# Kernel optimization log

Measured on AMD Instinct MI355X. Metric: run time of the kernel, lower is better.

## Reference

```python
import jax, jax.numpy as jnp
import numpy as np


def _conv1x1(x, w, b):
    # x: [B, Cin, H, W]; w: [Cout, Cin, 1, 1]; b: [Cout]
    y = jnp.einsum('bchw,oc->bohw', x, w[:, :, 0, 0])
    return y + b[None, :, None, None]


def setup_inputs() -> dict:
    key = jax.random.key(0)
    ks = jax.random.split(key, 9)
    B, C, H, W = 8, 256, 64, 64
    Cq = C // 4
    sc = 0.05
    return {
        'x': jax.random.normal(ks[0], (B, C, H, W), jnp.float32),
        'query_weight': jax.random.normal(ks[1], (Cq, C, 1, 1), jnp.float32) * sc,
        'query_bias': jax.random.normal(ks[2], (Cq,), jnp.float32) * sc,
        'key_weight': jax.random.normal(ks[3], (Cq, C, 1, 1), jnp.float32) * sc,
        'key_bias': jax.random.normal(ks[4], (Cq,), jnp.float32) * sc,
        'value_weight': jax.random.normal(ks[5], (C, C, 1, 1), jnp.float32) * sc,
        'value_bias': jax.random.normal(ks[6], (C,), jnp.float32) * sc,
        'gamma_weight': jax.random.normal(ks[7], (C, C, 1, 1), jnp.float32) * sc,
        'gamma_bias': jax.random.normal(ks[8], (C,), jnp.float32) * sc,
    }


def reference(x, query_weight, query_bias, key_weight, key_bias,
              value_weight, value_bias, gamma_weight, gamma_bias):
    B, C, H, W = x.shape
    N = H * W
    q = _conv1x1(x, query_weight, query_bias).reshape(B, -1, N)   # [B, Cq, N]
    k = _conv1x1(x, key_weight, key_bias).reshape(B, -1, N)       # [B, Cq, N]
    v = _conv1x1(x, value_weight, value_bias).reshape(B, C, N)    # [B, C, N]
    # energy[b, i, j] = sum_c q[b, c, i] * k[b, c, j]
    energy = jnp.einsum('bci,bcj->bij', q, k)                     # [B, N, N]
    energy = jax.nn.elu(energy) / N
    out = jnp.einsum('bcn,bnm->bcm', v, energy).reshape(B, C, H, W)
    return _conv1x1(out, gamma_weight, gamma_bias)
```

## Files before the change

### kernel.cpp

```cpp
#include <hip/hip_runtime.h>
#include <cmath>

#define BB 8
#define CC 256
#define CQ 64
#define NN 4096
constexpr float INV_N = 1.0f / 4096.0f;

typedef __attribute__((ext_vector_type(8))) short short8;
typedef __attribute__((ext_vector_type(4))) short short4v;
typedef __attribute__((ext_vector_type(4))) float float4v;

__device__ __forceinline__ short f2bf(float f) {
  union { float f; unsigned u; } x; x.f = f;
  unsigned r = x.u + 0x7fffu + ((x.u >> 16) & 1u);
  return (short)(r >> 16);
}

__device__ __forceinline__ void lds_barrier() {
  asm volatile("s_waitcnt lgkmcnt(0)" ::: "memory");
  __builtin_amdgcn_s_barrier();
  __builtin_amdgcn_sched_barrier(0);
}

__global__ void wconv_kernel(const float* __restrict__ wq,
                             const float* __restrict__ wk,
                             const float* __restrict__ wv,
                             const float* __restrict__ wg,
                             short* __restrict__ wqb, short* __restrict__ wkb,
                             short* __restrict__ wvb, short* __restrict__ wgb) {
  const int t = blockIdx.x * 256 + threadIdx.x;
  const float* src;
  short* dst;
  int idx;
  if (t < 4096)        { src = wq; dst = wqb; idx = t; }
  else if (t < 8192)   { src = wk; dst = wkb; idx = t - 4096; }
  else if (t < 24576)  { src = wv; dst = wvb; idx = t - 8192; }
  else                 { src = wg; dst = wgb; idx = t - 24576; }
  const float4 v = *reinterpret_cast<const float4*>(&src[(size_t)idx * 4]);
  short4v o;
  o[0] = f2bf(v.x); o[1] = f2bf(v.y); o[2] = f2bf(v.z); o[3] = f2bf(v.w);
  *reinterpret_cast<short4v*>(&dst[(size_t)idx * 4]) = o;
}

__global__ __launch_bounds__(256, 2) void qkv_kernel(
    const float* __restrict__ X,
    const short* __restrict__ wqb, const float* __restrict__ bq,
    const short* __restrict__ wkb, const float* __restrict__ bk,
    const short* __restrict__ wvb, const float* __restrict__ bv,
    short* __restrict__ qt, short* __restrict__ kt, short* __restrict__ vbf) {
  __shared__ short xt[64 * 264];
  const int tid = threadIdx.x;
  const int wid = tid >> 6;
  const int lane = tid & 63, quad = lane >> 4, l16 = lane & 15;
  const int b = blockIdx.x, n0 = blockIdx.y * 64;

  float4 xb[16];
#pragma unroll
  for (int p = 0; p < 16; ++p) {
    const int idx = p * 256 + tid;
    const int c = idx >> 4;
    const int n4 = (idx & 15) * 4;
    xb[p] = *reinterpret_cast<const float4*>(
        &X[((size_t)b * CC + c) * NN + n0 + n4]);
  }
#pragma unroll
  for (int p = 0; p < 16; ++p) {
    const int idx = p * 256 + tid;
    const int c = idx >> 4;
    const int n4 = (idx & 15) * 4;
    xt[(n4 + 0) * 264 + c] = f2bf(xb[p].x);
    xt[(n4 + 1) * 264 + c] = f2bf(xb[p].y);
    xt[(n4 + 2) * 264 + c] = f2bf(xb[p].z);
    xt[(n4 + 3) * 264 + c] = f2bf(xb[p].w);
  }
  __syncthreads();

  short8 bfr[8][4];
#pragma unroll
  for (int kk = 0; kk < 8; ++kk)
#pragma unroll
    for (int tm = 0; tm < 4; ++tm)
      bfr[kk][tm] = *reinterpret_cast<const short8*>(
          &xt[(tm * 16 + l16) * 264 + kk * 32 + quad * 8]);
  __syncthreads();

  short* Os0 = xt;
  short* Os1 = xt + 4608;

  for (int ch = 0; ch < 6; ++ch) {
    const short* W; const float* bias; int obase;
    if (ch == 0)      { W = wqb; bias = bq; obase = 0; }
    else if (ch == 1) { W = wkb; bias = bk; obase = 0; }
    else { W = wvb + (size_t)(ch - 2) * 64 * CC; bias = bv + (ch - 2) * 64; obase = (ch - 2) * 64; }

    const short* wrow = &W[(size_t)(wid * 16 + l16) * CC + quad * 8];
    short8 wf[8];
#pragma unroll
    for (int kk = 0; kk < 8; ++kk)
      wf[kk] = *reinterpret_cast<const short8*>(wrow + kk * 32);

    float4v acc[4];
#pragma unroll
    for (int tm = 0; tm < 4; ++tm) acc[tm] = float4v{0.f, 0.f, 0.f, 0.f};
#pragma unroll
    for (int kk = 0; kk < 8; ++kk)
#pragma unroll
      for (int tm = 0; tm < 4; ++tm)
        acc[tm] = __builtin_amdgcn_mfma_f32_16x16x32_bf16(wf[kk], bfr[kk][tm], acc[tm], 0, 0, 0);

    if (ch < 2) {
      short* dst = (ch == 0) ? qt : kt;
#pragma unroll
      for (int tm = 0; tm < 4; ++tm) {
        short4v pk;
#pragma unroll
        for (int r = 0; r < 4; ++r)
          pk[r] = f2bf(acc[tm][r] + bias[wid * 16 + quad * 4 + r]);
        *reinterpret_cast<short4v*>(
            &dst[((size_t)b * NN + n0 + tm * 16 + l16) * 64 + wid * 16 + quad * 4]) = pk;
      }
    } else {
      short* Os = (ch & 1) ? Os1 : Os0;
#pragma unroll
      for (int tm = 0; tm < 4; ++tm)
#pragma unroll
        for (int r = 0; r < 4; ++r)
          Os[(wid * 16 + quad * 4 + r) * 72 + tm * 16 + l16] =
              f2bf(acc[tm][r] + bias[wid * 16 + quad * 4 + r]);
      __syncthreads();
      const int o = tid >> 2, ng = (tid & 3) * 16;
      const short8 s0 = *reinterpret_cast<const short8*>(&Os[o * 72 + ng]);
      const short8 s1 = *reinterpret_cast<const short8*>(&Os[o * 72 + ng + 8]);
      short* vp = &vbf[((size_t)b * CC + obase + o) * NN + n0 + ng];
      *reinterpret_cast<short8*>(vp) = s0;
      *reinterpret_cast<short8*>(vp + 8) = s1;
    }
  }
}

__global__ __launch_bounds__(256, 2) void attn_kernel(
    const short* __restrict__ qt, const short* __restrict__ kt,
    const short* __restrict__ vbf, const short* __restrict__ wgb,
    const float* __restrict__ bg, float* __restrict__ out) {
  __shared__ short smem[16896];
  short* Es0 = smem;
  short* Es1 = smem + 4608;
  short* Outs = smem;

  const int tid = threadIdx.x;
  const int wid = tid >> 6;
  const int lane = tid & 63, quad = lane >> 4, l16 = lane & 15;
  const int b = blockIdx.x, m0 = blockIdx.y * 64;

  short8 bkf[4][2];
#pragma unroll
  for (int tm = 0; tm < 4; ++tm)
#pragma unroll
    for (int kk = 0; kk < 2; ++kk)
      bkf[tm][kk] = *reinterpret_cast<const short8*>(
          &kt[((size_t)b * NN + m0 + tm * 16 + l16) * 64 + kk * 32 + quad * 8]);

  const short* qp = &qt[((size_t)b * NN + wid * 16 + l16) * 64 + quad * 8];
  const short* vrow[4];
#pragma unroll
  for (int tc = 0; tc < 4; ++tc)
    vrow[tc] = &vbf[((size_t)b * CC + wid * 64 + tc * 16 + l16) * NN + quad * 8];

  float4v acc[4][4];
#pragma unroll
  for (int i = 0; i < 4; ++i)
#pragma unroll
    for (int j = 0; j < 4; ++j) acc[i][j] = float4v{0.f, 0.f, 0.f, 0.f};

  short8 avA[4][2], avB[4][2];
#pragma unroll
  for (int tc = 0; tc < 4; ++tc) {
    avA[tc][0] = *reinterpret_cast<const short8*>(vrow[tc]);
    avA[tc][1] = *reinterpret_cast<const short8*>(vrow[tc] + 32);
  }
  short8 aqA0 = *reinterpret_cast<const short8*>(qp + (size_t)1 * 4096);
  short8 aqA1 = *reinterpret_cast<const short8*>(qp + (size_t)1 * 4096 + 32);
  short8 aqB0, aqB1;
  {
    const short8 aq0 = *reinterpret_cast<const short8*>(qp);
    const short8 aq1 = *reinterpret_cast<const short8*>(qp + 32);
#pragma unroll
    for (int tm = 0; tm < 4; ++tm) {
      float4v t = {0.f, 0.f, 0.f, 0.f};
      t = __builtin_amdgcn_mfma_f32_16x16x32_bf16(aq0, bkf[tm][0], t, 0, 0, 0);
      t = __builtin_amdgcn_mfma_f32_16x16x32_bf16(aq1, bkf[tm][1], t, 0, 0, 0);
      short4v pk;
#pragma unroll
      for (int r = 0; r < 4; ++r) {
        float sv = t[r];
        sv = (sv > 0.f) ? sv : (__expf(sv) - 1.f);
        pk[r] = f2bf(sv);
      }
      *reinterpret_cast<short4v*>(
          &Es0[(tm * 16 + l16) * 72 + wid * 16 + quad * 4]) = pk;
    }
  }
  lds_barrier();

  auto seg = [&](int it, short8 (&avc)[4][2], short8 (&avn)[4][2],
                 short8& aqc0, short8& aqc1, short8& aqn0, short8& aqn1) {
    const int nb1 = (it + 1) * 64;
#pragma unroll
    for (int tc = 0; tc < 4; ++tc) {
      avn[tc][0] = *reinterpret_cast<const short8*>(vrow[tc] + nb1);
      avn[tc][1] = *reinterpret_cast<const short8*>(vrow[tc] + nb1 + 32);
    }
    aqn0 = *reinterpret_cast<const short8*>(qp + (size_t)(it + 2) * 4096);
    aqn1 = *reinterpret_cast<const short8*>(qp + (size_t)(it + 2) * 4096 + 32);

    short* Esr = (it & 1) ? Es1 : Es0;
    short* Esw = (it & 1) ? Es0 : Es1;

    float4v s[4];
    if (it < 63) {
#pragma unroll
      for (int tm = 0; tm < 4; ++tm) {
        float4v t = {0.f, 0.f, 0.f, 0.f};
        t = __builtin_amdgcn_mfma_f32_16x16x32_bf16(aqc0, bkf[tm][0], t, 0, 0, 0);
        t = __builtin_amdgcn_mfma_f32_16x16x32_bf16(aqc1, bkf[tm][1], t, 0, 0, 0);
        s[tm] = t;
      }
    }

#pragma unroll
    for (int tm = 0; tm < 4; ++tm) {
      const short8 be0 = *reinterpret_cast<const short8*>(
          &Esr[(tm * 16 + l16) * 72 + quad * 8]);
      const short8 be1 = *reinterpret_cast<const short8*>(
          &Esr[(tm * 16 + l16) * 72 + 32 + quad * 8]);
#pragma unroll
      for (int tc = 0; tc < 4; ++tc) {
        acc[tc][tm] = __builtin_amdgcn_mfma_f32_16x16x32_bf16(avc[tc][0], be0, acc[tc][tm], 0, 0, 0);
        acc[tc][tm] = __builtin_amdgcn_mfma_f32_16x16x32_bf16(avc[tc][1], be1, acc[tc][tm], 0, 0, 0);
      }
    }

    if (it < 63) {
#pragma unroll
      for (int tm = 0; tm < 4; ++tm) {
        short4v pk;
#pragma unroll
        for (int r = 0; r < 4; ++r) {
          float sv = s[tm][r];
          sv = (sv > 0.f) ? sv : (__expf(sv) - 1.f);
          pk[r] = f2bf(sv);
        }
        *reinterpret_cast<short4v*>(
            &Esw[(tm * 16 + l16) * 72 + wid * 16 + quad * 4]) = pk;
      }
    }
    lds_barrier();
  };

  for (int it = 0; it < 64; it += 2) {
    seg(it,     avA, avB, aqA0, aqA1, aqB0, aqB1);
    seg(it + 1, avB, avA, aqB0, aqB1, aqA0, aqA1);
  }

#pragma unroll
  for (int tc = 0; tc < 4; ++tc)
#pragma unroll
    for (int tm = 0; tm < 4; ++tm) {
      short4v pk;
#pragma unroll
      for (int r = 0; r < 4; ++r) pk[r] = f2bf(acc[tc][tm][r] * INV_N);
      *reinterpret_cast<short4v*>(
          &Outs[(tm * 16 + l16) * 264 + wid * 64 + tc * 16 + quad * 4]) = pk;
    }
  __syncthreads();

#pragma unroll
  for (int i = 0; i < 4; ++i)
#pragma unroll
    for (int j = 0; j < 4; ++j) acc[i][j] = float4v{0.f, 0.f, 0.f, 0.f};

  for (int ks8 = 0; ks8 < 8; ++ks8) {
    short8 ag[4];
#pragma unroll
    for (int to = 0; to < 4; ++to)
      ag[to] = *reinterpret_cast<const short8*>(
          &wgb[(size_t)(wid * 64 + to * 16 + l16) * CC + ks8 * 32 + quad * 8]);
    short8 bo[4];
#pragma unroll
    for (int tm = 0; tm < 4; ++tm)
      bo[tm] = *reinterpret_cast<const short8*>(
          &Outs[(tm * 16 + l16) * 264 + ks8 * 32 + quad * 8]);
#pragma unroll
    for (int to = 0; to < 4; ++to)
#pragma unroll
      for (int tm = 0; tm < 4; ++tm)
        acc[to][tm] =
            __builtin_amdgcn_mfma_f32_16x16x32_bf16(ag[to], bo[tm], acc[to][tm], 0, 0, 0);
  }

#pragma unroll
  for (int to = 0; to < 4; ++to) {
#pragma unroll
    for (int r = 0; r < 4; ++r) {
      const int o = wid * 64 + to * 16 + quad * 4 + r;
      const float bgv = bg[o];
#pragma unroll
      for (int tm = 0; tm < 4; ++tm) {
        out[((size_t)b * CC + o) * NN + m0 + tm * 16 + l16] =
            acc[to][tm][r] + bgv;
      }
    }
  }
}

extern "C" void kernel_launch(void* const* d_in, const int* in_sizes, int n_in,
                              void* d_out, int out_size, void* d_ws,
                              size_t ws_size, hipStream_t stream) {
  const float* x  = (const float*)d_in[0];
  const float* wq = (const float*)d_in[1];
  const float* bq = (const float*)d_in[2];
  const float* wk = (const float*)d_in[3];
  const float* bk = (const float*)d_in[4];
  const float* wv = (const float*)d_in[5];
  const float* bv = (const float*)d_in[6];
  const float* wg = (const float*)d_in[7];
  const float* bg = (const float*)d_in[8];
  float* out = (float*)d_out;

  short* qt  = (short*)d_ws;
  short* kt  = qt + (size_t)BB * NN * CQ;
  short* vbf = kt + (size_t)BB * NN * CQ;
  short* wqb = vbf + (size_t)BB * CC * NN;
  short* wkb = wqb + (size_t)CQ * CC;
  short* wvb = wkb + (size_t)CQ * CC;
  short* wgb = wvb + (size_t)CC * CC;

  wconv_kernel<<<dim3(160), 256, 0, stream>>>(wq, wk, wv, wg, wqb, wkb, wvb, wgb);
  qkv_kernel<<<dim3(BB, NN / 64), 256, 0, stream>>>(x, wqb, bq, wkb, bk, wvb, bv,
                                                    qt, kt, vbf);
  attn_kernel<<<dim3(BB, NN / 64), 256, 0, stream>>>(qt, kt, vbf, wgb, bg, out);
}
```

Measured before the change: 270.0 us.

## Fold gamma projection into value weights and pad V row stride

Precomputes Wg·Wv and Wg·bv in a new prep kernel so the value projection directly produces gamma-projected values. This removes the trailing 1x1 gamma GEMM and its LDS staging from the attention kernel, leaving only scaling and bias at output. The V buffer row stride is also padded to 4224 to reduce memory conflicts on strided row reads. It adds a small extra launch and changes rounding because the combined weight is quantised to bf16.

Measured after the change: 274.7 us. About the same (+1.7%).

```diff
diff --git a/kernel.cpp b/kernel.cpp
--- a/kernel.cpp
+++ b/kernel.cpp
@@ -5,6 +5,7 @@
 #define CC 256
 #define CQ 64
 #define NN 4096
+#define VROW 4224
 constexpr float INV_N = 1.0f / 4096.0f;
 
 typedef __attribute__((ext_vector_type(8))) short short8;
@@ -25,29 +26,42 @@
 
 __global__ void wconv_kernel(const float* __restrict__ wq,
                              const float* __restrict__ wk,
-                             const float* __restrict__ wv,
-                             const float* __restrict__ wg,
-                             short* __restrict__ wqb, short* __restrict__ wkb,
-                             short* __restrict__ wvb, short* __restrict__ wgb) {
+                             short* __restrict__ wqb, short* __restrict__ wkb) {
   const int t = blockIdx.x * 256 + threadIdx.x;
-  const float* src;
-  short* dst;
-  int idx;
-  if (t < 4096)        { src = wq; dst = wqb; idx = t; }
-  else if (t < 8192)   { src = wk; dst = wkb; idx = t - 4096; }
-  else if (t < 24576)  { src = wv; dst = wvb; idx = t - 8192; }
-  else                 { src = wg; dst = wgb; idx = t - 24576; }
+  const float* src; short* dst; int idx;
+  if (t < 4096) { src = wq; dst = wqb; idx = t; }
+  else          { src = wk; dst = wkb; idx = t - 4096; }
   const float4 v = *reinterpret_cast<const float4*>(&src[(size_t)idx * 4]);
   short4v o;
   o[0] = f2bf(v.x); o[1] = f2bf(v.y); o[2] = f2bf(v.z); o[3] = f2bf(v.w);
   *reinterpret_cast<short4v*>(&dst[(size_t)idx * 4]) = o;
 }
 
+__global__ void wprep_kernel(const float* __restrict__ wg,
+                             const float* __restrict__ wv,
+                             const float* __restrict__ bv,
+                             short* __restrict__ wvpb, float* __restrict__ bvp) {
+  const int o = blockIdx.x, t = threadIdx.x;
+  float s = 0.f;
+  for (int c = 0; c < 256; ++c)
+    s += wg[(size_t)o * 256 + c] * wv[(size_t)c * 256 + t];
+  wvpb[(size_t)o * 256 + t] = f2bf(s);
+
+  __shared__ float red[256];
+  red[t] = wg[(size_t)o * 256 + t] * bv[t];
+  __syncthreads();
+  for (int off = 128; off; off >>= 1) {
+    if (t < off) red[t] += red[t + off];
+    __syncthreads();
+  }
+  if (t == 0) bvp[o] = red[0];
+}
+
 __global__ __launch_bounds__(256, 2) void qkv_kernel(
     const float* __restrict__ X,
     const short* __restrict__ wqb, const float* __restrict__ bq,
     const short* __restrict__ wkb, const float* __restrict__ bk,
-    const short* __restrict__ wvb, const float* __restrict__ bv,
+    const short* __restrict__ wvpb, const float* __restrict__ bvp,
     short* __restrict__ qt, short* __restrict__ kt, short* __restrict__ vbf) {
   __shared__ short xt[64 * 264];
   const int tid = threadIdx.x;
@@ -92,7 +106,7 @@
     const short* W; const float* bias; int obase;
     if (ch == 0)      { W = wqb; bias = bq; obase = 0; }
     else if (ch == 1) { W = wkb; bias = bk; obase = 0; }
-    else { W = wvb + (size_t)(ch - 2) * 64 * CC; bias = bv + (ch - 2) * 64; obase = (ch - 2) * 64; }
+    else { W = wvpb + (size_t)(ch - 2) * 64 * CC; bias = bvp + (ch - 2) * 64; obase = (ch - 2) * 64; }
 
     const short* wrow = &W[(size_t)(wid * 16 + l16) * CC + quad * 8];
     short8 wf[8];
@@ -130,9 +144,10 @@
               f2bf(acc[tm][r] + bias[wid * 16 + quad * 4 + r]);
       __syncthreads();
       const int o = tid >> 2, ng = (tid & 3) * 16;
+      const int orow = obase + o;
       const short8 s0 = *reinterpret_cast<const short8*>(&Os[o * 72 + ng]);
       const short8 s1 = *reinterpret_cast<const short8*>(&Os[o * 72 + ng + 8]);
-      short* vp = &vbf[((size_t)b * CC + obase + o) * NN + n0 + ng];
+      short* vp = &vbf[((size_t)b * CC + orow) * VROW + n0 + ng];
       *reinterpret_cast<short8*>(vp) = s0;
       *reinterpret_cast<short8*>(vp + 8) = s1;
     }
@@ -141,12 +156,11 @@
 
 __global__ __launch_bounds__(256, 2) void attn_kernel(
     const short* __restrict__ qt, const short* __restrict__ kt,
-    const short* __restrict__ vbf, const short* __restrict__ wgb,
-    const float* __restrict__ bg, float* __restrict__ out) {
-  __shared__ short smem[16896];
+    const short* __restrict__ vbf, const float* __restrict__ bg,
+    float* __restrict__ out) {
+  __shared__ short smem[9216];
   short* Es0 = smem;
   short* Es1 = smem + 4608;
-  short* Outs = smem;
 
   const int tid = threadIdx.x;
   const int wid = tid >> 6;
@@ -164,8 +178,10 @@
   const short* qp = &qt[((size_t)b * NN + wid * 16 + l16) * 64 + quad * 8];
   const short* vrow[4];
 #pragma unroll
-  for (int tc = 0; tc < 4; ++tc)
-    vrow[tc] = &vbf[((size_t)b * CC + wid * 64 + tc * 16 + l16) * NN + quad * 8];
+  for (int tc = 0; tc < 4; ++tc) {
+    const int crow = wid * 64 + tc * 16 + l16;
+    vrow[tc] = &vbf[((size_t)b * CC + crow) * VROW + quad * 8];
+  }
 
   float4v acc[4][4];
 #pragma unroll
@@ -264,51 +280,15 @@
   }
 
 #pragma unroll
-  for (int tc = 0; tc < 4; ++tc)
-#pragma unroll
-    for (int tm = 0; tm < 4; ++tm) {
-      short4v pk;
-#pragma unroll
-      for (int r = 0; r < 4; ++r) pk[r] = f2bf(acc[tc][tm][r] * INV_N);
-      *reinterpret_cast<short4v*>(
-          &Outs[(tm * 16 + l16) * 264 + wid * 64 + tc * 16 + quad * 4]) = pk;
-    }
-  __syncthreads();
-
-#pragma unroll
-  for (int i = 0; i < 4; ++i)
-#pragma unroll
-    for (int j = 0; j < 4; ++j) acc[i][j] = float4v{0.f, 0.f, 0.f, 0.f};
-
-  for (int ks8 = 0; ks8 < 8; ++ks8) {
-    short8 ag[4];
-#pragma unroll
-    for (int to = 0; to < 4; ++to)
-      ag[to] = *reinterpret_cast<const short8*>(
-          &wgb[(size_t)(wid * 64 + to * 16 + l16) * CC + ks8 * 32 + quad * 8]);
-    short8 bo[4];
-#pragma unroll
-    for (int tm = 0; tm < 4; ++tm)
-      bo[tm] = *reinterpret_cast<const short8*>(
-          &Outs[(tm * 16 + l16) * 264 + ks8 * 32 + quad * 8]);
-#pragma unroll
-    for (int to = 0; to < 4; ++to)
-#pragma unroll
-      for (int tm = 0; tm < 4; ++tm)
-        acc[to][tm] =
-            __builtin_amdgcn_mfma_f32_16x16x32_bf16(ag[to], bo[tm], acc[to][tm], 0, 0, 0);
-  }
-
-#pragma unroll
-  for (int to = 0; to < 4; ++to) {
+  for (int tc = 0; tc < 4; ++tc) {
 #pragma unroll
     for (int r = 0; r < 4; ++r) {
-      const int o = wid * 64 + to * 16 + quad * 4 + r;
+      const int o = wid * 64 + tc * 16 + quad * 4 + r;
       const float bgv = bg[o];
 #pragma unroll
       for (int tm = 0; tm < 4; ++tm) {
         out[((size_t)b * CC + o) * NN + m0 + tm * 16 + l16] =
-            acc[to][tm][r] + bgv;
+            acc[tc][tm][r] * INV_N + bgv;
       }
     }
   }
@@ -328,16 +308,17 @@
   const float* bg = (const float*)d_in[8];
   float* out = (float*)d_out;
 
-  short* qt  = (short*)d_ws;
-  short* kt  = qt + (size_t)BB * NN * CQ;
-  short* vbf = kt + (size_t)BB * NN * CQ;
-  short* wqb = vbf + (size_t)BB * CC * NN;
-  short* wkb = wqb + (size_t)CQ * CC;
-  short* wvb = wkb + (size_t)CQ * CC;
-  short* wgb = wvb + (size_t)CC * CC;
-
-  wconv_kernel<<<dim3(160), 256, 0, stream>>>(wq, wk, wv, wg, wqb, wkb, wvb, wgb);
-  qkv_kernel<<<dim3(BB, NN / 64), 256, 0, stream>>>(x, wqb, bq, wkb, bk, wvb, bv,
-                                                    qt, kt, vbf);
-  attn_kernel<<<dim3(BB, NN / 64), 256, 0, stream>>>(qt, kt, vbf, wgb, bg, out);
-}
+  short* qt   = (short*)d_ws;
+  short* kt   = qt + (size_t)BB * NN * CQ;
+  short* vbf  = kt + (size_t)BB * NN * CQ;
+  short* wqb  = vbf + (size_t)BB * CC * VROW;
+  short* wkb  = wqb + (size_t)CQ * CC;
+  short* wvpb = wkb + (size_t)CQ * CC;
+  float* bvp  = (float*)(wvpb + (size_t)CC * CC);
+
+  wconv_kernel<<<dim3(32), 256, 0, stream>>>(wq, wk, wqb, wkb);
+  wprep_kernel<<<dim3(256), 256, 0, stream>>>(wg, wv, bv, wvpb, bvp);
+  qkv_kernel<<<dim3(BB, NN / 64), 256, 0, stream>>>(x, wqb, bq, wkb, bk,
+                                                    wvpb, bvp, qt, kt, vbf);
+  attn_kernel<<<dim3(BB, NN / 64), 256, 0, stream>>>(qt, kt, vbf, bg, out);
+}
```
